# Kernel tuning notes

Measured on AMD Instinct MI355X. Metric: run time of the kernel, lower is better.

The kernel has to match this reference:

```python
import jax, jax.numpy as jnp
import numpy as np

K = 5            # kernel_size for gaussian and bilateral
PAD = K // 2
SIGMA = 1.0          # gaussian sigma / bilateral sigma_spatial
SIGMA_INT = 0.1      # bilateral sigma_intensity


def _spatial_kernel():
    coords = jnp.arange(K, dtype=jnp.float32) - K // 2
    x, y = jnp.meshgrid(coords, coords, indexing='ij')
    return jnp.exp(-(x ** 2 + y ** 2) / (2.0 * SIGMA ** 2))  # (K, K), unnormalized


def setup_inputs() -> dict:
    key = jax.random.key(0)
    images = jax.random.uniform(key, (8, 3, 512, 512), dtype=jnp.float32)
    return {"images": images}


def _gaussian_filter(images):
    g = _spatial_kernel()
    g = g / g.sum()
    kernel = jnp.tile(g[None, None], (3, 1, 1, 1))  # (3,1,K,K) depthwise
    return jax.lax.conv_general_dilated(
        images, kernel, window_strides=(1, 1),
        padding=[(PAD, PAD), (PAD, PAD)],
        dimension_numbers=('NCHW', 'OIHW', 'NCHW'),
        feature_group_count=3)


def _bilateral_filter(images):
    B, C, H, W = images.shape
    padded = jnp.pad(images, ((0, 0), (0, 0), (PAD, PAD), (PAD, PAD)), mode='reflect')
    # im2col: (B, C, K*K, H, W) -- fixed 25-iteration loop over kernel offsets
    patches = jnp.stack([padded[:, :, i:i + H, j:j + W]
                         for i in range(K) for j in range(K)], axis=2)
    center = patches[:, :, K * K // 2:K * K // 2 + 1]  # (B,C,1,H,W)
    iw = jnp.exp(-(patches - center) ** 2 / (2.0 * SIGMA_INT ** 2))
    sw = _spatial_kernel().reshape(1, 1, K * K, 1, 1)
    w = sw * iw
    w = w / (w.sum(axis=2, keepdims=True) + 1e-8)
    return (patches * w).sum(axis=2)  # (B,C,H,W)


def reference(images):
    # AdaptiveAntiAlias.forward(images, mode='auto')
    gaussian_out = _gaussian_filter(images)
    bilateral_out = _bilateral_filter(images)
    return 0.6 * gaussian_out + 0.4 * bilateral_out
```

## Files before the change

kernel.cpp:

```cpp
#include <hip/hip_runtime.h>

#define IMG_H 512
#define IMG_W 512
#define HW    (IMG_H * IMG_W)
#define NCH   24

__device__ __forceinline__ float fexp2(float x) {
#if __has_builtin(__builtin_amdgcn_exp2f)
    return __builtin_amdgcn_exp2f(x);
#else
    float r; asm("v_exp_f32 %0, %1" : "=v"(r) : "v"(x)); return r;
#endif
}
__device__ __forceinline__ float frcp(float x) {
#if __has_builtin(__builtin_amdgcn_rcpf)
    return __builtin_amdgcn_rcpf(x);
#else
    float r; asm("v_rcp_f32 %0, %1" : "=v"(r) : "v"(x)); return r;
#endif
}

__device__ __forceinline__ constexpr double exs(int r2) {
    return (r2 == 0) ? 1.0
         : (r2 == 1) ? 0.60653065971263342
         : (r2 == 2) ? 0.36787944117144233
         : (r2 == 4) ? 0.13533528323661270
         : (r2 == 5) ? 0.08208499862389880
         : (r2 == 8) ? 0.01831563888873418 : 0.0;
}
#define SSUM 6.16892408102888092
__device__ __forceinline__ constexpr float k1(int d)  { return (float)exs(d * d); }
__device__ __forceinline__ constexpr float k1n(int d) { return (float)(exs(d * d) / SSUM); }
#define NEG50  -72.134752044448169f
#define LG     -0.72134752044448169f

#define PER_CH_B (4 * 128 + 508 * 2)
#define N_B (PER_CH_B * NCH)
#define XT 126
#define YT 127
#define PER_CH_T (XT * YT)
#define N_INT (PER_CH_T * NCH)
#define N_TOTAL (N_B + N_INT)

__device__ __constant__ const int c_unused = 0;

__global__ __launch_bounds__(256) void aa_kernel(const float* __restrict__ in,
                                                 float* __restrict__ out) {
    const int gid = blockIdx.x * 256 + threadIdx.x;

    if (gid < N_B) {
        const int ch = gid / PER_CH_B;
        const int r  = gid - ch * PER_CH_B;
        int y, x0;
        if (r < 512) {
            const int q = r >> 7;
            y  = (q < 2) ? q : q + 508;
            x0 = (r & 127) << 2;
        } else {
            const int t = r - 512;
            y  = 2 + (t >> 1);
            x0 = (t & 1) ? (IMG_W - 4) : 0;
        }
        const float* __restrict__ img = in + ch * HW;

        int ry[5]; float krow[5];
        #pragma unroll
        for (int i = 0; i < 5; ++i) {
            const int yy = y + i - 2;
            const int ryy = (yy < 0) ? -yy : ((yy >= IMG_H) ? 2 * IMG_H - 2 - yy : yy);
            ry[i] = ryy * IMG_W;
            krow[i] = ((yy >= 0) & (yy < IMG_H)) ? k1(i - 2) : 0.0f;
        }
        int rx[8]; float xin[8];
        #pragma unroll
        for (int c = 0; c < 8; ++c) {
            const int xx = x0 + c - 2;
            rx[c] = (xx < 0) ? -xx : ((xx >= IMG_W) ? 2 * IMG_W - 2 - xx : xx);
            xin[c] = ((xx >= 0) & (xx < IMG_W)) ? 1.0f : 0.0f;
        }
        float v[5][8];
        #pragma unroll
        for (int i = 0; i < 5; ++i) {
            #pragma unroll
            for (int c = 0; c < 8; ++c) v[i][c] = img[ry[i] + rx[c]];
        }

        float csm[8];
        #pragma unroll
        for (int c = 0; c < 8; ++c) {
            float s = krow[0] * v[0][c];
            s = fmaf(krow[1], v[1][c], s);
            s = fmaf(krow[2], v[2][c], s);
            s = fmaf(krow[3], v[3][c], s);
            s = fmaf(krow[4], v[4][c], s);
            csm[c] = s * xin[c];
        }

        float res[4];
        #pragma unroll
        for (int p = 0; p < 4; ++p) {
            const float ctr = v[2][2 + p];
            float arg[24];
            {
                int t = 0;
                #pragma unroll
                for (int i = 0; i < 5; ++i) {
                    #pragma unroll
                    for (int j = 0; j < 5; ++j) {
                        if (i == 2 && j == 2) continue;
                        const int r2 = (i - 2) * (i - 2) + (j - 2) * (j - 2);
                        const float d = v[i][p + j] - ctr;
                        arg[t] = fmaf(d * d, NEG50, LG * (float)r2);
                        ++t;
                    }
                }
            }
            float w[24];
            #pragma unroll
            for (int k = 0; k < 24; ++k) w[k] = fexp2(arg[k]);

            float ws0 = 1.0f, ws1 = 0.f, ws2 = 0.f, ws3 = 0.f;
            float bs0 = ctr,  bs1 = 0.f, bs2 = 0.f, bs3 = 0.f;
            {
                int t = 0;
                #pragma unroll
                for (int i = 0; i < 5; ++i) {
                    #pragma unroll
                    for (int j = 0; j < 5; ++j) {
                        if (i == 2 && j == 2) continue;
                        const float vv = v[i][p + j];
                        if ((t & 3) == 0)      { ws0 += w[t]; bs0 = fmaf(w[t], vv, bs0); }
                        else if ((t & 3) == 1) { ws1 += w[t]; bs1 = fmaf(w[t], vv, bs1); }
                        else if ((t & 3) == 2) { ws2 += w[t]; bs2 = fmaf(w[t], vv, bs2); }
                        else                   { ws3 += w[t]; bs3 = fmaf(w[t], vv, bs3); }
                        ++t;
                    }
                }
            }
            const float wsum = (ws0 + ws1) + (ws2 + ws3);
            const float bsum = (bs0 + bs1) + (bs2 + bs3);

            float g = k1n(2) * csm[p];
            g = fmaf(k1n(1), csm[p + 1], g);
            g = fmaf(k1n(0), csm[p + 2], g);
            g = fmaf(k1n(1), csm[p + 3], g);
            g = fmaf(k1n(2), csm[p + 4], g);

            res[p] = fmaf(0.6f, g, 0.4f * (bsum * frcp(wsum + 1e-8f)));
        }

        float4* o4 = (float4*)(out + ch * HW + y * IMG_W + x0);
        *o4 = make_float4(res[0], res[1], res[2], res[3]);
    } else {
        const int ig = gid - N_B;
        if (ig >= N_INT) return;
        const int ch  = ig / PER_CH_T;
        const int rem = ig - ch * PER_CH_T;
        const int ty  = rem / XT;
        const int y0  = 2 + ty * 4;
        const int x0  = 4 + (rem - ty * XT) * 4;

        const float* __restrict__ img = in + ch * HW;
        const float* base = img + (y0 - 2) * IMG_W + (x0 - 2);

        float v[8][8];
        #pragma unroll
        for (int r = 0; r < 8; ++r) {
            const float2* rp = (const float2*)(base + r * IMG_W);
            #pragma unroll
            for (int c = 0; c < 4; ++c) {
                const float2 t = rp[c];
                v[r][2 * c]     = t.x;
                v[r][2 * c + 1] = t.y;
            }
        }

        float ws[16], bs[16];
        #pragma unroll
        for (int p = 0; p < 16; ++p) {
            const int pr = p >> 2, pc = p & 3;
            ws[p] = 1.0f;
            bs[p] = v[pr + 2][pc + 2];
        }

        constexpr int PDI[12] = {0, 0, 1,  1, 1, 1, 1, 2,  2, 2, 2, 2};
        constexpr int PDJ[12] = {1, 2, -2, -1, 0, 1, 2, -2, -1, 0, 1, 2};

        #pragma unroll
        for (int o = 0; o < 12; ++o) {
            const int di = PDI[o], dj = PDJ[o];
            const int r2 = di * di + dj * dj;
            const float lsw = LG * (float)r2;
            float wt[16];
            #pragma unroll
            for (int p = 0; p < 16; ++p) {
                const int pr = p >> 2, pc = p & 3;
                const float d = v[pr + 2 + di][pc + 2 + dj] - v[pr + 2][pc + 2];
                wt[p] = fexp2(fmaf(d * d, NEG50, lsw));
            }
            #pragma unroll
            for (int p = 0; p < 16; ++p) {
                const int pr = p >> 2, pc = p & 3;
                const float vp = v[pr + 2][pc + 2];
                const float vt = v[pr + 2 + di][pc + 2 + dj];
                ws[p] += wt[p];
                bs[p] = fmaf(wt[p], vt, bs[p]);
                const int qr = pr + di, qc = pc + dj;
                if (qr >= 0 && qr < 4 && qc >= 0 && qc < 4) {
                    const int q = qr * 4 + qc;
                    ws[q] += wt[p];
                    bs[q] = fmaf(wt[p], vp, bs[q]);
                }
            }
        }
        #pragma unroll
        for (int o = 0; o < 12; ++o) {
            const int di = -PDI[o], dj = -PDJ[o];
            const int r2 = di * di + dj * dj;
            const float lsw = LG * (float)r2;
            float wt[16];
            #pragma unroll
            for (int p = 0; p < 16; ++p) {
                const int pr = p >> 2, pc = p & 3;
                const int qr = pr + di, qc = pc + dj;
                if (qr < 0 || qr >= 4 || qc < 0 || qc >= 4) {
                    const float d = v[pr + 2 + di][pc + 2 + dj] - v[pr + 2][pc + 2];
                    wt[p] = fexp2(fmaf(d * d, NEG50, lsw));
                }
            }
            #pragma unroll
            for (int p = 0; p < 16; ++p) {
                const int pr = p >> 2, pc = p & 3;
                const int qr = pr + di, qc = pc + dj;
                if (qr < 0 || qr >= 4 || qc < 0 || qc >= 4) {
                    const float vt = v[pr + 2 + di][pc + 2 + dj];
                    ws[p] += wt[p];
                    bs[p] = fmaf(wt[p], vt, bs[p]);
                }
            }
        }

        float cs[4][8];
        #pragma unroll
        for (int yr = 0; yr < 4; ++yr) {
            #pragma unroll
            for (int c = 0; c < 8; ++c) {
                float s = k1(2) * v[yr][c];
                s = fmaf(k1(1), v[yr + 1][c], s);
                s = fmaf(k1(0), v[yr + 2][c], s);
                s = fmaf(k1(1), v[yr + 3][c], s);
                s = fmaf(k1(2), v[yr + 4][c], s);
                cs[yr][c] = s;
            }
        }

        float* op = out + ch * HW + y0 * IMG_W + x0;
        #pragma unroll
        for (int yr = 0; yr < 4; ++yr) {
            float res[4];
            #pragma unroll
            for (int pc = 0; pc < 4; ++pc) {
                float g = k1n(2) * cs[yr][pc];
                g = fmaf(k1n(1), cs[yr][pc + 1], g);
                g = fmaf(k1n(0), cs[yr][pc + 2], g);
                g = fmaf(k1n(1), cs[yr][pc + 3], g);
                g = fmaf(k1n(2), cs[yr][pc + 4], g);
                const int p = yr * 4 + pc;
                res[pc] = fmaf(0.6f, g, 0.4f * (bs[p] * frcp(ws[p] + 1e-8f)));
            }
            *(float4*)(op + yr * IMG_W) = make_float4(res[0], res[1], res[2], res[3]);
        }
    }
}

extern "C" void kernel_launch(void* const* d_in, const int* in_sizes, int n_in,
                              void* d_out, int out_size, void* d_ws, size_t ws_size,
                              hipStream_t stream) {
    const float* img = (const float*)d_in[0];
    float* out = (float*)d_out;
    const int blocks = (N_TOTAL + 255) / 256;
    aa_kernel<<<blocks, 256, 0, stream>>>(img, out);
}
```

Baseline: 38.95 us.

## Process two vertically stacked 4x4 tiles per thread, reusing overlapping halo rows

Interior threads now compute two consecutive 4x4 output tiles in a non-unrolled loop. For the second tile, the 4 overlapping input rows are shifted in registers and only 4 new rows are loaded. A remainder path handles the last row of tiles with a single tile per thread. This halves the interior thread count and cuts redundant halo loads, at the cost of lower parallelism and a serial dependency inside each thread.

```diff
diff --git a/kernel.cpp b/kernel.cpp
--- a/kernel.cpp
+++ b/kernel.cpp
@@ -37,12 +37,12 @@
 #define PER_CH_B (4 * 128 + 508 * 2)
 #define N_B (PER_CH_B * NCH)
 #define XT 126
-#define YT 127
-#define PER_CH_T (XT * YT)
-#define N_INT (PER_CH_T * NCH)
-#define N_TOTAL (N_B + N_INT)
-
-__device__ __constant__ const int c_unused = 0;
+#define KY 63
+#define PER_CH_M (XT * KY)
+#define N_MAIN (PER_CH_M * NCH)
+#define PER_CH_R XT
+#define N_REM (PER_CH_R * NCH)
+#define N_TOTAL (N_B + N_MAIN + N_REM)
 
 __global__ __launch_bounds__(256) void aa_kernel(const float* __restrict__ in,
                                                  float* __restrict__ out) {
@@ -153,12 +153,22 @@
         *o4 = make_float4(res[0], res[1], res[2], res[3]);
     } else {
         const int ig = gid - N_B;
-        if (ig >= N_INT) return;
-        const int ch  = ig / PER_CH_T;
-        const int rem = ig - ch * PER_CH_T;
-        const int ty  = rem / XT;
-        const int y0  = 2 + ty * 4;
-        const int x0  = 4 + (rem - ty * XT) * 4;
+        int ch, x0, y0, ntiles;
+        if (ig < N_MAIN) {
+            ch = ig / PER_CH_M;
+            const int rem = ig - ch * PER_CH_M;
+            const int ky = rem / XT;
+            y0 = 2 + 8 * ky;
+            x0 = 4 + (rem - ky * XT) * 4;
+            ntiles = 2;
+        } else {
+            const int ir = ig - N_MAIN;
+            if (ir >= N_REM) return;
+            ch = ir / PER_CH_R;
+            x0 = 4 + (ir - ch * PER_CH_R) * 4;
+            y0 = 506;
+            ntiles = 1;
+        }
 
         const float* __restrict__ img = in + ch * HW;
         const float* base = img + (y0 - 2) * IMG_W + (x0 - 2);
@@ -175,100 +185,123 @@
             }
         }
 
-        float ws[16], bs[16];
-        #pragma unroll
-        for (int p = 0; p < 16; ++p) {
-            const int pr = p >> 2, pc = p & 3;
-            ws[p] = 1.0f;
-            bs[p] = v[pr + 2][pc + 2];
-        }
-
-        constexpr int PDI[12] = {0, 0, 1,  1, 1, 1, 1, 2,  2, 2, 2, 2};
-        constexpr int PDJ[12] = {1, 2, -2, -1, 0, 1, 2, -2, -1, 0, 1, 2};
-
-        #pragma unroll
-        for (int o = 0; o < 12; ++o) {
-            const int di = PDI[o], dj = PDJ[o];
-            const int r2 = di * di + dj * dj;
-            const float lsw = LG * (float)r2;
-            float wt[16];
+        float* op = out + ch * HW + y0 * IMG_W + x0;
+
+        #pragma unroll 1
+        for (int t = 0; t < ntiles; ++t) {
+            if (t) {
+                #pragma unroll
+                for (int r = 0; r < 4; ++r) {
+                    #pragma unroll
+                    for (int c = 0; c < 8; ++c) v[r][c] = v[r + 4][c];
+                }
+                #pragma unroll
+                for (int r = 4; r < 8; ++r) {
+                    const float2* rp = (const float2*)(base + (r + 4) * IMG_W);
+                    #pragma unroll
+                    for (int c = 0; c < 4; ++c) {
+                        const float2 tt = rp[c];
+                        v[r][2 * c]     = tt.x;
+                        v[r][2 * c + 1] = tt.y;
+                    }
+                }
+            }
+
+            float ws[16], bs[16];
             #pragma unroll
             for (int p = 0; p < 16; ++p) {
                 const int pr = p >> 2, pc = p & 3;
-                const float d = v[pr + 2 + di][pc + 2 + dj] - v[pr + 2][pc + 2];
-                wt[p] = fexp2(fmaf(d * d, NEG50, lsw));
-            }
-            #pragma unroll
-            for (int p = 0; p < 16; ++p) {
-                const int pr = p >> 2, pc = p & 3;
-                const float vp = v[pr + 2][pc + 2];
-                const float vt = v[pr + 2 + di][pc + 2 + dj];
-                ws[p] += wt[p];
-                bs[p] = fmaf(wt[p], vt, bs[p]);
-                const int qr = pr + di, qc = pc + dj;
-                if (qr >= 0 && qr < 4 && qc >= 0 && qc < 4) {
-                    const int q = qr * 4 + qc;
-                    ws[q] += wt[p];
-                    bs[q] = fmaf(wt[p], vp, bs[q]);
-                }
-            }
-        }
-        #pragma unroll
-        for (int o = 0; o < 12; ++o) {
-            const int di = -PDI[o], dj = -PDJ[o];
-            const int r2 = di * di + dj * dj;
-            const float lsw = LG * (float)r2;
-            float wt[16];
-            #pragma unroll
-            for (int p = 0; p < 16; ++p) {
-                const int pr = p >> 2, pc = p & 3;
-                const int qr = pr + di, qc = pc + dj;
-                if (qr < 0 || qr >= 4 || qc < 0 || qc >= 4) {
+                ws[p] = 1.0f;
+                bs[p] = v[pr + 2][pc + 2];
+            }
+
+            constexpr int PDI[12] = {0, 0, 1,  1, 1, 1, 1, 2,  2, 2, 2, 2};
+            constexpr int PDJ[12] = {1, 2, -2, -1, 0, 1, 2, -2, -1, 0, 1, 2};
+
+            #pragma unroll
+            for (int o = 0; o < 12; ++o) {
+                const int di = PDI[o], dj = PDJ[o];
+                const int r2 = di * di + dj * dj;
+                const float lsw = LG * (float)r2;
+                float wt[16];
+                #pragma unroll
+                for (int p = 0; p < 16; ++p) {
+                    const int pr = p >> 2, pc = p & 3;
                     const float d = v[pr + 2 + di][pc + 2 + dj] - v[pr + 2][pc + 2];
                     wt[p] = fexp2(fmaf(d * d, NEG50, lsw));
                 }
-            }
-            #pragma unroll
-            for (int p = 0; p < 16; ++p) {
-                const int pr = p >> 2, pc = p & 3;
-                const int qr = pr + di, qc = pc + dj;
-                if (qr < 0 || qr >= 4 || qc < 0 || qc >= 4) {
+                #pragma unroll
+                for (int p = 0; p < 16; ++p) {
+                    const int pr = p >> 2, pc = p & 3;
+                    const float vp = v[pr + 2][pc + 2];
                     const float vt = v[pr + 2 + di][pc + 2 + dj];
                     ws[p] += wt[p];
                     bs[p] = fmaf(wt[p], vt, bs[p]);
-                }
-            }
-        }
-
-        float cs[4][8];
-        #pragma unroll
-        for (int yr = 0; yr < 4; ++yr) {
-            #pragma unroll
-            for (int c = 0; c < 8; ++c) {
-                float s = k1(2) * v[yr][c];
-                s = fmaf(k1(1), v[yr + 1][c], s);
-                s = fmaf(k1(0), v[yr + 2][c], s);
-                s = fmaf(k1(1), v[yr + 3][c], s);
-                s = fmaf(k1(2), v[yr + 4][c], s);
-                cs[yr][c] = s;
-            }
-        }
-
-        float* op = out + ch * HW + y0 * IMG_W + x0;
-        #pragma unroll
-        for (int yr = 0; yr < 4; ++yr) {
-            float res[4];
-            #pragma unroll
-            for (int pc = 0; pc < 4; ++pc) {
-                float g = k1n(2) * cs[yr][pc];
-                g = fmaf(k1n(1), cs[yr][pc + 1], g);
-                g = fmaf(k1n(0), cs[yr][pc + 2], g);
-                g = fmaf(k1n(1), cs[yr][pc + 3], g);
-                g = fmaf(k1n(2), cs[yr][pc + 4], g);
-                const int p = yr * 4 + pc;
-                res[pc] = fmaf(0.6f, g, 0.4f * (bs[p] * frcp(ws[p] + 1e-8f)));
-            }
-            *(float4*)(op + yr * IMG_W) = make_float4(res[0], res[1], res[2], res[3]);
+                    const int qr = pr + di, qc = pc + dj;
+                    if (qr >= 0 && qr < 4 && qc >= 0 && qc < 4) {
+                        const int q = qr * 4 + qc;
+                        ws[q] += wt[p];
+                        bs[q] = fmaf(wt[p], vp, bs[q]);
+                    }
+                }
+            }
+            #pragma unroll
+            for (int o = 0; o < 12; ++o) {
+                const int di = -PDI[o], dj = -PDJ[o];
+                const int r2 = di * di + dj * dj;
+                const float lsw = LG * (float)r2;
+                float wt[16];
+                #pragma unroll
+                for (int p = 0; p < 16; ++p) {
+                    const int pr = p >> 2, pc = p & 3;
+                    const int qr = pr + di, qc = pc + dj;
+                    if (qr < 0 || qr >= 4 || qc < 0 || qc >= 4) {
+                        const float d = v[pr + 2 + di][pc + 2 + dj] - v[pr + 2][pc + 2];
+                        wt[p] = fexp2(fmaf(d * d, NEG50, lsw));
+                    }
+                }
+                #pragma unroll
+                for (int p = 0; p < 16; ++p) {
+                    const int pr = p >> 2, pc = p & 3;
+                    const int qr = pr + di, qc = pc + dj;
+                    if (qr < 0 || qr >= 4 || qc < 0 || qc >= 4) {
+                        const float vt = v[pr + 2 + di][pc + 2 + dj];
+                        ws[p] += wt[p];
+                        bs[p] = fmaf(wt[p], vt, bs[p]);
+                    }
+                }
+            }
+
+            float cs[4][8];
+            #pragma unroll
+            for (int yr = 0; yr < 4; ++yr) {
+                #pragma unroll
+                for (int c = 0; c < 8; ++c) {
+                    float s = k1(2) * v[yr][c];
+                    s = fmaf(k1(1), v[yr + 1][c], s);
+                    s = fmaf(k1(0), v[yr + 2][c], s);
+                    s = fmaf(k1(1), v[yr + 3][c], s);
+                    s = fmaf(k1(2), v[yr + 4][c], s);
+                    cs[yr][c] = s;
+                }
+            }
+
+            float* opt = op + t * 4 * IMG_W;
+            #pragma unroll
+            for (int yr = 0; yr < 4; ++yr) {
+                float res[4];
+                #pragma unroll
+                for (int pc = 0; pc < 4; ++pc) {
+                    float g = k1n(2) * cs[yr][pc];
+                    g = fmaf(k1n(1), cs[yr][pc + 1], g);
+                    g = fmaf(k1n(0), cs[yr][pc + 2], g);
+                    g = fmaf(k1n(1), cs[yr][pc + 3], g);
+                    const int p = yr * 4 + pc;
+                    g = fmaf(k1n(2), cs[yr][pc + 4], g);
+                    res[pc] = fmaf(0.6f, g, 0.4f * (bs[p] * frcp(ws[p] + 1e-8f)));
+                }
+                *(float4*)(opt + yr * IMG_W) = make_float4(res[0], res[1], res[2], res[3]);
+            }
         }
     }
 }
```

Result: slower. 44.73 us (+14.8%).

## Stage reflect-padded 64x64 tiles in LDS and unify border and interior paths

Applied to the files above, without the earlier changes.

Each block now loads a reflect-padded 68x68 tile of one channel into shared memory, resolving reflection at load time. Every thread then reads its 8x8 neighbourhood from LDS and runs the symmetric 4x4 bilateral/gaussian path, so the separate border path with scalar reflected global loads goes away. This trades per-thread global float2 loads, whose overlap was left to the cache, for one cooperative tile load plus a barrier. It also adds LDS traffic and possible bank conflicts on the float4 reads.

```diff
diff --git a/kernel.cpp b/kernel.cpp
--- a/kernel.cpp
+++ b/kernel.cpp
@@ -1,9 +1,10 @@
 #include <hip/hip_runtime.h>
 
-#define IMG_H 512
-#define IMG_W 512
-#define HW    (IMG_H * IMG_W)
+#define IMG   512
+#define HW    (IMG * IMG)
 #define NCH   24
+#define LDSW  68
+#define LDSN  (LDSW * LDSW)
 
 __device__ __forceinline__ float fexp2(float x) {
 #if __has_builtin(__builtin_amdgcn_exp2f)
@@ -34,242 +35,145 @@
 #define NEG50  -72.134752044448169f
 #define LG     -0.72134752044448169f
 
-#define PER_CH_B (4 * 128 + 508 * 2)
-#define N_B (PER_CH_B * NCH)
-#define XT 126
-#define YT 127
-#define PER_CH_T (XT * YT)
-#define N_INT (PER_CH_T * NCH)
-#define N_TOTAL (N_B + N_INT)
-
-__device__ __constant__ const int c_unused = 0;
-
 __global__ __launch_bounds__(256) void aa_kernel(const float* __restrict__ in,
                                                  float* __restrict__ out) {
-    const int gid = blockIdx.x * 256 + threadIdx.x;
+    __shared__ float sm[LDSN];
 
-    if (gid < N_B) {
-        const int ch = gid / PER_CH_B;
-        const int r  = gid - ch * PER_CH_B;
-        int y, x0;
-        if (r < 512) {
-            const int q = r >> 7;
-            y  = (q < 2) ? q : q + 508;
-            x0 = (r & 127) << 2;
-        } else {
-            const int t = r - 512;
-            y  = 2 + (t >> 1);
-            x0 = (t & 1) ? (IMG_W - 4) : 0;
+    const int bid = blockIdx.x;
+    const int ch  = bid >> 6;
+    const int b2  = bid & 63;
+    const int by  = b2 >> 3, bx = b2 & 7;
+    const int y0b = by * 64, x0b = bx * 64;
+    const float* __restrict__ img = in + ch * HW;
+    const int tid = threadIdx.x;
+
+    for (int idx = tid; idx < LDSN; idx += 256) {
+        const int lr = idx / LDSW;
+        const int lc = idx - lr * LDSW;
+        int gr = y0b + lr - 2;
+        int gc = x0b + lc - 2;
+        gr = (gr < 0) ? -gr : ((gr >= IMG) ? 2 * IMG - 2 - gr : gr);
+        gc = (gc < 0) ? -gc : ((gc >= IMG) ? 2 * IMG - 2 - gc : gc);
+        sm[idx] = img[gr * IMG + gc];
+    }
+    __syncthreads();
+
+    const int tr = tid >> 4, tc = tid & 15;
+    const int py = y0b + tr * 4;
+    const int px = x0b + tc * 4;
+
+    float v[8][8];
+    #pragma unroll
+    for (int r = 0; r < 8; ++r) {
+        const float4* p0 = (const float4*)&sm[(tr * 4 + r) * LDSW + tc * 4];
+        const float4 a = p0[0], b = p0[1];
+        v[r][0] = a.x; v[r][1] = a.y; v[r][2] = a.z; v[r][3] = a.w;
+        v[r][4] = b.x; v[r][5] = b.y; v[r][6] = b.z; v[r][7] = b.w;
+    }
+
+    float ws[16], bs[16];
+    #pragma unroll
+    for (int p = 0; p < 16; ++p) {
+        const int pr = p >> 2, pc = p & 3;
+        ws[p] = 1.0f;
+        bs[p] = v[pr + 2][pc + 2];
+    }
+
+    constexpr int PDI[12] = {0, 0, 1,  1, 1, 1, 1, 2,  2, 2, 2, 2};
+    constexpr int PDJ[12] = {1, 2, -2, -1, 0, 1, 2, -2, -1, 0, 1, 2};
+
+    #pragma unroll
+    for (int o = 0; o < 12; ++o) {
+        const int di = PDI[o], dj = PDJ[o];
+        const int r2 = di * di + dj * dj;
+        const float lsw = LG * (float)r2;
+        float wt[16];
+        #pragma unroll
+        for (int p = 0; p < 16; ++p) {
+            const int pr = p >> 2, pc = p & 3;
+            const float d = v[pr + 2 + di][pc + 2 + dj] - v[pr + 2][pc + 2];
+            wt[p] = fexp2(fmaf(d * d, NEG50, lsw));
         }
-        const float* __restrict__ img = in + ch * HW;
+        #pragma unroll
+        for (int p = 0; p < 16; ++p) {
+            const int pr = p >> 2, pc = p & 3;
+            const float vp = v[pr + 2][pc + 2];
+            const float vt = v[pr + 2 + di][pc + 2 + dj];
+            ws[p] += wt[p];
+            bs[p] = fmaf(wt[p], vt, bs[p]);
+            const int qr = pr + di, qc = pc + dj;
+            if (qr >= 0 && qr < 4 && qc >= 0 && qc < 4) {
+                const int q = qr * 4 + qc;
+                ws[q] += wt[p];
+                bs[q] = fmaf(wt[p], vp, bs[q]);
+            }
+        }
+    }
+    #pragma unroll
+    for (int o = 0; o < 12; ++o) {
+        const int di = -PDI[o], dj = -PDJ[o];
+        const int r2 = di * di + dj * dj;
+        const float lsw = LG * (float)r2;
+        float wt[16];
+        #pragma unroll
+        for (int p = 0; p < 16; ++p) {
+            const int pr = p >> 2, pc = p & 3;
+            const int qr = pr + di, qc = pc + dj;
+            if (qr < 0 || qr >= 4 || qc < 0 || qc >= 4) {
+                const float d = v[pr + 2 + di][pc + 2 + dj] - v[pr + 2][pc + 2];
+                wt[p] = fexp2(fmaf(d * d, NEG50, lsw));
+            }
+        }
+        #pragma unroll
+        for (int p = 0; p < 16; ++p) {
+            const int pr = p >> 2, pc = p & 3;
+            const int qr = pr + di, qc = pc + dj;
+            if (qr < 0 || qr >= 4 || qc < 0 || qc >= 4) {
+                const float vt = v[pr + 2 + di][pc + 2 + dj];
+                ws[p] += wt[p];
+                bs[p] = fmaf(wt[p], vt, bs[p]);
+            }
+        }
+    }
 
-        int ry[5]; float krow[5];
+    float xin[8];
+    #pragma unroll
+    for (int c = 0; c < 8; ++c) {
+        const int gx = px + c - 2;
+        xin[c] = ((gx >= 0) & (gx < IMG)) ? 1.0f : 0.0f;
+    }
+
+    float* op = out + ch * HW + py * IMG + px;
+    #pragma unroll
+    for (int yr = 0; yr < 4; ++yr) {
+        float kr[5];
         #pragma unroll
         for (int i = 0; i < 5; ++i) {
-            const int yy = y + i - 2;
-            const int ryy = (yy < 0) ? -yy : ((yy >= IMG_H) ? 2 * IMG_H - 2 - yy : yy);
-            ry[i] = ryy * IMG_W;
-            krow[i] = ((yy >= 0) & (yy < IMG_H)) ? k1(i - 2) : 0.0f;
+            const int gy = py + yr + i - 2;
+            kr[i] = ((gy >= 0) & (gy < IMG)) ? k1(i - 2) : 0.0f;
         }
-        int rx[8]; float xin[8];
-        #pragma unroll
-        for (int c = 0; c < 8; ++c) {
-            const int xx = x0 + c - 2;
-            rx[c] = (xx < 0) ? -xx : ((xx >= IMG_W) ? 2 * IMG_W - 2 - xx : xx);
-            xin[c] = ((xx >= 0) & (xx < IMG_W)) ? 1.0f : 0.0f;
-        }
-        float v[5][8];
-        #pragma unroll
-        for (int i = 0; i < 5; ++i) {
-            #pragma unroll
-            for (int c = 0; c < 8; ++c) v[i][c] = img[ry[i] + rx[c]];
-        }
-
         float csm[8];
         #pragma unroll
         for (int c = 0; c < 8; ++c) {
-            float s = krow[0] * v[0][c];
-            s = fmaf(krow[1], v[1][c], s);
-            s = fmaf(krow[2], v[2][c], s);
-            s = fmaf(krow[3], v[3][c], s);
-            s = fmaf(krow[4], v[4][c], s);
+            float s = kr[0] * v[yr][c];
+            s = fmaf(kr[1], v[yr + 1][c], s);
+            s = fmaf(kr[2], v[yr + 2][c], s);
+            s = fmaf(kr[3], v[yr + 3][c], s);
+            s = fmaf(kr[4], v[yr + 4][c], s);
             csm[c] = s * xin[c];
         }
-
         float res[4];
         #pragma unroll
-        for (int p = 0; p < 4; ++p) {
-            const float ctr = v[2][2 + p];
-            float arg[24];
-            {
-                int t = 0;
-                #pragma unroll
-                for (int i = 0; i < 5; ++i) {
-                    #pragma unroll
-                    for (int j = 0; j < 5; ++j) {
-                        if (i == 2 && j == 2) continue;
-                        const int r2 = (i - 2) * (i - 2) + (j - 2) * (j - 2);
-                        const float d = v[i][p + j] - ctr;
-                        arg[t] = fmaf(d * d, NEG50, LG * (float)r2);
-                        ++t;
-                    }
-                }
-            }
-            float w[24];
-            #pragma unroll
-            for (int k = 0; k < 24; ++k) w[k] = fexp2(arg[k]);
-
-            float ws0 = 1.0f, ws1 = 0.f, ws2 = 0.f, ws3 = 0.f;
-            float bs0 = ctr,  bs1 = 0.f, bs2 = 0.f, bs3 = 0.f;
-            {
-                int t = 0;
-                #pragma unroll
-                for (int i = 0; i < 5; ++i) {
-                    #pragma unroll
-                    for (int j = 0; j < 5; ++j) {
-                        if (i == 2 && j == 2) continue;
-                        const float vv = v[i][p + j];
-                        if ((t & 3) == 0)      { ws0 += w[t]; bs0 = fmaf(w[t], vv, bs0); }
-                        else if ((t & 3) == 1) { ws1 += w[t]; bs1 = fmaf(w[t], vv, bs1); }
-                        else if ((t & 3) == 2) { ws2 += w[t]; bs2 = fmaf(w[t], vv, bs2); }
-                        else                   { ws3 += w[t]; bs3 = fmaf(w[t], vv, bs3); }
-                        ++t;
-                    }
-                }
-            }
-            const float wsum = (ws0 + ws1) + (ws2 + ws3);
-            const float bsum = (bs0 + bs1) + (bs2 + bs3);
-
-            float g = k1n(2) * csm[p];
-            g = fmaf(k1n(1), csm[p + 1], g);
-            g = fmaf(k1n(0), csm[p + 2], g);
-            g = fmaf(k1n(1), csm[p + 3], g);
-            g = fmaf(k1n(2), csm[p + 4], g);
-
-            res[p] = fmaf(0.6f, g, 0.4f * (bsum * frcp(wsum + 1e-8f)));
+        for (int pc = 0; pc < 4; ++pc) {
+            float g = k1n(2) * csm[pc];
+            g = fmaf(k1n(1), csm[pc + 1], g);
+            g = fmaf(k1n(0), csm[pc + 2], g);
+            g = fmaf(k1n(1), csm[pc + 3], g);
+            g = fmaf(k1n(2), csm[pc + 4], g);
+            const int p = yr * 4 + pc;
+            res[pc] = fmaf(0.6f, g, 0.4f * (bs[p] * frcp(ws[p] + 1e-8f)));
         }
-
-        float4* o4 = (float4*)(out + ch * HW + y * IMG_W + x0);
-        *o4 = make_float4(res[0], res[1], res[2], res[3]);
-    } else {
-        const int ig = gid - N_B;
-        if (ig >= N_INT) return;
-        const int ch  = ig / PER_CH_T;
-        const int rem = ig - ch * PER_CH_T;
-        const int ty  = rem / XT;
-        const int y0  = 2 + ty * 4;
-        const int x0  = 4 + (rem - ty * XT) * 4;
-
-        const float* __restrict__ img = in + ch * HW;
-        const float* base = img + (y0 - 2) * IMG_W + (x0 - 2);
-
-        float v[8][8];
-        #pragma unroll
-        for (int r = 0; r < 8; ++r) {
-            const float2* rp = (const float2*)(base + r * IMG_W);
-            #pragma unroll
-            for (int c = 0; c < 4; ++c) {
-                const float2 t = rp[c];
-                v[r][2 * c]     = t.x;
-                v[r][2 * c + 1] = t.y;
-            }
-        }
-
-        float ws[16], bs[16];
-        #pragma unroll
-        for (int p = 0; p < 16; ++p) {
-            const int pr = p >> 2, pc = p & 3;
-            ws[p] = 1.0f;
-            bs[p] = v[pr + 2][pc + 2];
-        }
-
-        constexpr int PDI[12] = {0, 0, 1,  1, 1, 1, 1, 2,  2, 2, 2, 2};
-        constexpr int PDJ[12] = {1, 2, -2, -1, 0, 1, 2, -2, -1, 0, 1, 2};
-
-        #pragma unroll
-        for (int o = 0; o < 12; ++o) {
-            const int di = PDI[o], dj = PDJ[o];
-            const int r2 = di * di + dj * dj;
-            const float lsw = LG * (float)r2;
-            float wt[16];
-            #pragma unroll
-            for (int p = 0; p < 16; ++p) {
-                const int pr = p >> 2, pc = p & 3;
-                const float d = v[pr + 2 + di][pc + 2 + dj] - v[pr + 2][pc + 2];
-                wt[p] = fexp2(fmaf(d * d, NEG50, lsw));
-            }
-            #pragma unroll
-            for (int p = 0; p < 16; ++p) {
-                const int pr = p >> 2, pc = p & 3;
-                const float vp = v[pr + 2][pc + 2];
-                const float vt = v[pr + 2 + di][pc + 2 + dj];
-                ws[p] += wt[p];
-                bs[p] = fmaf(wt[p], vt, bs[p]);
-                const int qr = pr + di, qc = pc + dj;
-                if (qr >= 0 && qr < 4 && qc >= 0 && qc < 4) {
-                    const int q = qr * 4 + qc;
-                    ws[q] += wt[p];
-                    bs[q] = fmaf(wt[p], vp, bs[q]);
-                }
-            }
-        }
-        #pragma unroll
-        for (int o = 0; o < 12; ++o) {
-            const int di = -PDI[o], dj = -PDJ[o];
-            const int r2 = di * di + dj * dj;
-            const float lsw = LG * (float)r2;
-            float wt[16];
-            #pragma unroll
-            for (int p = 0; p < 16; ++p) {
-                const int pr = p >> 2, pc = p & 3;
-                const int qr = pr + di, qc = pc + dj;
-                if (qr < 0 || qr >= 4 || qc < 0 || qc >= 4) {
-                    const float d = v[pr + 2 + di][pc + 2 + dj] - v[pr + 2][pc + 2];
-                    wt[p] = fexp2(fmaf(d * d, NEG50, lsw));
-                }
-            }
-            #pragma unroll
-            for (int p = 0; p < 16; ++p) {
-                const int pr = p >> 2, pc = p & 3;
-                const int qr = pr + di, qc = pc + dj;
-                if (qr < 0 || qr >= 4 || qc < 0 || qc >= 4) {
-                    const float vt = v[pr + 2 + di][pc + 2 + dj];
-                    ws[p] += wt[p];
-                    bs[p] = fmaf(wt[p], vt, bs[p]);
-                }
-            }
-        }
-
-        float cs[4][8];
-        #pragma unroll
-        for (int yr = 0; yr < 4; ++yr) {
-            #pragma unroll
-            for (int c = 0; c < 8; ++c) {
-                float s = k1(2) * v[yr][c];
-                s = fmaf(k1(1), v[yr + 1][c], s);
-                s = fmaf(k1(0), v[yr + 2][c], s);
-                s = fmaf(k1(1), v[yr + 3][c], s);
-                s = fmaf(k1(2), v[yr + 4][c], s);
-                cs[yr][c] = s;
-            }
-        }
-
-        float* op = out + ch * HW + y0 * IMG_W + x0;
-        #pragma unroll
-        for (int yr = 0; yr < 4; ++yr) {
-            float res[4];
-            #pragma unroll
-            for (int pc = 0; pc < 4; ++pc) {
-                float g = k1n(2) * cs[yr][pc];
-                g = fmaf(k1n(1), cs[yr][pc + 1], g);
-                g = fmaf(k1n(0), cs[yr][pc + 2], g);
-                g = fmaf(k1n(1), cs[yr][pc + 3], g);
-                g = fmaf(k1n(2), cs[yr][pc + 4], g);
-                const int p = yr * 4 + pc;
-                res[pc] = fmaf(0.6f, g, 0.4f * (bs[p] * frcp(ws[p] + 1e-8f)));
-            }
-            *(float4*)(op + yr * IMG_W) = make_float4(res[0], res[1], res[2], res[3]);
-        }
+        *(float4*)(op + yr * IMG) = make_float4(res[0], res[1], res[2], res[3]);
     }
 }
 
@@ -278,6 +182,5 @@
                               hipStream_t stream) {
     const float* img = (const float*)d_in[0];
     float* out = (float*)d_out;
-    const int blocks = (N_TOTAL + 255) / 256;
-    aa_kernel<<<blocks, 256, 0, stream>>>(img, out);
+    aa_kernel<<<NCH * 64, 256, 0, stream>>>(img, out);
 }
```

New measurement: 41.28 us. 6.0% more time.
